# Kernel optimization log

Measured on AMD Instinct MI355X. Metric: run time of the kernel, lower is better.

The kernel has to match this reference:

```python
import jax, jax.numpy as jnp
import numpy as np

EXP_CLAMP = 1.0e6
DENOM_EPS = 1e-10
LRELU_ALPHA = 0.01


def setup_inputs() -> dict:
    key = jax.random.key(0)
    k1, k2, k3, k4, k5, k6 = jax.random.split(key, 6)
    B, N, E, F = 4, 16384, 262144, 64
    h = jax.random.normal(k1, (B, N, F), dtype=jnp.float32)
    edge = jax.random.randint(k2, (B, E, 2), 0, N, dtype=jnp.int32)
    edge_num = jax.random.randint(k3, (B,), 1, E, dtype=jnp.int32)
    edge_weight = jax.random.uniform(k4, (B, E), dtype=jnp.float32)
    W = jax.random.normal(k5, (F, F), dtype=jnp.float32) * 0.15  # xavier-ish scale
    a = jax.random.normal(k6, (1, 2 * F), dtype=jnp.float32) * 0.12
    return {"h": h, "edge": edge, "edge_num": edge_num,
            "edge_weight": edge_weight, "W": W, "a": a}


def _seg_sum(src, idx, num_segments):
    # src: [E, ...], idx: [E] -> [num_segments, ...]
    return jax.ops.segment_sum(src, idx, num_segments=num_segments)


def reference(h, edge, edge_num, edge_weight, W, a):
    B, N, Fin = h.shape
    E = edge.shape[1]
    # linear transform: Wh = h @ W^T  -> [B, N, Fout]
    Wh = jnp.einsum('bnf,of->bno', h, W)
    ctr = edge[:, :, 0]  # [B, E]
    nbr = edge[:, :, 1]  # [B, E]
    Wh_c = jnp.take_along_axis(Wh, ctr[:, :, None], axis=1)  # [B, E, Fout]
    Wh_n = jnp.take_along_axis(Wh, nbr[:, :, None], axis=1)  # [B, E, Fout]
    a_input = jnp.concatenate([Wh_c, Wh_n], axis=-1) * edge_weight[:, :, None]
    # attention logits: leakyrelu(a_input @ a^T), squeeze to [B, E]
    att1 = jax.nn.leaky_relu(jnp.einsum('bek,k->be', a_input, a[0]), LRELU_ALPHA)
    # per-batch valid-edge mask (edges beyond edge_num zeroed, as in torch loop)
    mask = (jnp.arange(E, dtype=jnp.int32)[None, :] < edge_num[:, None])
    x_exp = jnp.clip(jnp.exp(att1), 0.0, EXP_CLAMP) * mask.astype(att1.dtype)
    # segment softmax denominator over center nodes
    denom = DENOM_EPS + jax.vmap(_seg_sum, in_axes=(0, 0, None))(x_exp, ctr, N)  # [B, N]
    att = x_exp / jnp.take_along_axis(denom, ctr, axis=1)  # [B, E]
    # weighted neighbor aggregation via scatter-add on center index
    att_Wh = Wh_n * att[:, :, None]  # masked edges already have att == 0
    h_prime = jax.vmap(_seg_sum, in_axes=(0, 0, None))(att_Wh, ctr, N)  # [B, N, Fout]
    return jax.nn.relu(h_prime)
```

## Files before the change

### kernel.cpp

```cpp
#include <hip/hip_runtime.h>

#define BB 4
#define NN 16384
#define EE 262144
#define FF 64
#define ROWS (BB * NN)
#define CAP 64
#define CHUNKS 64
#define CHUNK_E (EE / CHUNKS)
#define TILE_R 256

typedef __bf16 bf16x8 __attribute__((ext_vector_type(8)));
typedef float  f32x4  __attribute__((ext_vector_type(4)));

__device__ __forceinline__ unsigned short f32_to_bf16(float f) {
    unsigned int u = __float_as_uint(f);
    u += 0x7FFFu + ((u >> 16) & 1u);
    return (unsigned short)(u >> 16);
}

__global__ __launch_bounds__(256) void mfma_kernel(
    const float* __restrict__ h, const float* __restrict__ W,
    const float* __restrict__ a,
    unsigned short* __restrict__ Wh,
    float* __restrict__ sc, float* __restrict__ sn)
{
    __shared__ float wc[FF], wn[FF];
    const int t = threadIdx.x;
    const int lane = t & 63;
    const int m = lane & 15;
    const int q = lane >> 4;

    if (t < 128) {
        const int f = t & 63;
        const float* av = a + (t >> 6) * FF;
        float s = 0.0f;
        #pragma unroll 8
        for (int o = 0; o < FF; ++o)
            s = fmaf(av[o], W[o * FF + f], s);
        (t < 64 ? wc : wn)[f] = s;
    }

    bf16x8 bfrag[4][2];
    #pragma unroll
    for (int nt = 0; nt < 4; ++nt) {
        const float* wr = W + (nt * 16 + m) * FF;
        #pragma unroll
        for (int kh = 0; kh < 2; ++kh) {
            const float4 v0 = *(const float4*)(wr + kh * 32 + q * 8);
            const float4 v1 = *(const float4*)(wr + kh * 32 + q * 8 + 4);
            bf16x8 b;
            b[0] = (__bf16)v0.x; b[1] = (__bf16)v0.y;
            b[2] = (__bf16)v0.z; b[3] = (__bf16)v0.w;
            b[4] = (__bf16)v1.x; b[5] = (__bf16)v1.y;
            b[6] = (__bf16)v1.z; b[7] = (__bf16)v1.w;
            bfrag[nt][kh] = b;
        }
    }

    __syncthreads();

    const int waveId = (blockIdx.x * 256 + t) >> 6;
    const int R0 = waveId * 16;
    const float* hr = h + (size_t)(R0 + m) * FF;
    bf16x8 af[2];
    float s1 = 0.0f, s2 = 0.0f;
    #pragma unroll
    for (int kh = 0; kh < 2; ++kh) {
        const float4 v0 = *(const float4*)(hr + kh * 32 + q * 8);
        const float4 v1 = *(const float4*)(hr + kh * 32 + q * 8 + 4);
        bf16x8 aa;
        aa[0] = (__bf16)v0.x; aa[1] = (__bf16)v0.y;
        aa[2] = (__bf16)v0.z; aa[3] = (__bf16)v0.w;
        aa[4] = (__bf16)v1.x; aa[5] = (__bf16)v1.y;
        aa[6] = (__bf16)v1.z; aa[7] = (__bf16)v1.w;
        af[kh] = aa;
        const int fb = kh * 32 + q * 8;
        const float4 c0 = *(const float4*)&wc[fb];
        const float4 c1 = *(const float4*)&wc[fb + 4];
        const float4 n0 = *(const float4*)&wn[fb];
        const float4 n1 = *(const float4*)&wn[fb + 4];
        s1 = fmaf(v0.x, c0.x, fmaf(v0.y, c0.y, fmaf(v0.z, c0.z, fmaf(v0.w, c0.w, s1))));
        s1 = fmaf(v1.x, c1.x, fmaf(v1.y, c1.y, fmaf(v1.z, c1.z, fmaf(v1.w, c1.w, s1))));
        s2 = fmaf(v0.x, n0.x, fmaf(v0.y, n0.y, fmaf(v0.z, n0.z, fmaf(v0.w, n0.w, s2))));
        s2 = fmaf(v1.x, n1.x, fmaf(v1.y, n1.y, fmaf(v1.z, n1.z, fmaf(v1.w, n1.w, s2))));
    }
    s1 += __shfl_xor(s1, 16); s2 += __shfl_xor(s2, 16);
    s1 += __shfl_xor(s1, 32); s2 += __shfl_xor(s2, 32);
    if (lane < 16) { sc[R0 + m] = s1; sn[R0 + m] = s2; }

    #pragma unroll
    for (int nt = 0; nt < 4; ++nt) {
        f32x4 acc = {0.f, 0.f, 0.f, 0.f};
        acc = __builtin_amdgcn_mfma_f32_16x16x32_bf16(af[0], bfrag[nt][0], acc, 0, 0, 0);
        acc = __builtin_amdgcn_mfma_f32_16x16x32_bf16(af[1], bfrag[nt][1], acc, 0, 0, 0);
        #pragma unroll
        for (int i = 0; i < 4; ++i)
            Wh[(size_t)(R0 + q * 4 + i) * FF + nt * 16 + m] = f32_to_bf16(acc[i]);
    }
}

__global__ __launch_bounds__(1024) void hist_kernel(
    const int* __restrict__ edge, const int* __restrict__ edge_num,
    unsigned short* __restrict__ histG)
{
    __shared__ unsigned int hist[NN];
    const int g = blockIdx.x;
    const int b = g >> 6, c = g & (CHUNKS - 1);
    const int t = threadIdx.x;
    const int en = edge_num[b];
    const int e0 = c * CHUNK_E;
    if (e0 >= en) return;

    for (int r = t; r < NN; r += 1024) hist[r] = 0u;
    __syncthreads();

    const int2* ep = (const int2*)edge + (size_t)b * EE + e0;
    const int nAct = min(en - e0, CHUNK_E);
    for (int j = t; j < nAct; j += 1024)
        atomicAdd(&hist[ep[j].x], 1u);
    __syncthreads();

    ushort2* out2 = (ushort2*)(histG + (size_t)g * NN);
    for (int r2 = t; r2 < NN / 2; r2 += 1024) {
        ushort2 v;
        v.x = (unsigned short)hist[2 * r2];
        v.y = (unsigned short)hist[2 * r2 + 1];
        out2[r2] = v;
    }
}

__global__ __launch_bounds__(256) void scan_kernel(
    const int* __restrict__ edge_num,
    unsigned short* __restrict__ histG, int* __restrict__ cnt)
{
    __shared__ unsigned short tile[CHUNKS][TILE_R];
    const int g = blockIdx.x;
    const int b = g >> 6, tl = g & 63;
    const int r0 = tl * TILE_R;
    const int t = threadIdx.x;
    const int en = edge_num[b];
    const int nact = min((en + CHUNK_E - 1) / CHUNK_E, CHUNKS);

    for (int c = 0; c < nact; ++c)
        tile[c][t] = histG[(size_t)(b * CHUNKS + c) * NN + r0 + t];
    __syncthreads();

    unsigned int acc = 0;
    for (int c = 0; c < nact; ++c) {
        const unsigned int v = tile[c][t];
        tile[c][t] = (unsigned short)(acc > 65535u ? 65535u : acc);
        acc += v;
    }
    cnt[b * NN + r0 + t] = (int)acc;

    for (int c = 0; c < nact; ++c)
        histG[(size_t)(b * CHUNKS + c) * NN + r0 + t] = tile[c][t];
}

__global__ __launch_bounds__(1024) void scatter_kernel(
    const int* __restrict__ edge, const int* __restrict__ edge_num,
    const unsigned short* __restrict__ baseG,
    const float* __restrict__ sc, const float* __restrict__ sn,
    const float* __restrict__ ew,
    unsigned int* __restrict__ payload)
{
    __shared__ unsigned int slotA[NN];
    const int g = blockIdx.x;
    const int b = g >> 6, c = g & (CHUNKS - 1);
    const int t = threadIdx.x;
    const int en = edge_num[b];
    const int e0 = c * CHUNK_E;
    if (e0 >= en) return;

    const ushort2* b2 = (const ushort2*)(baseG + (size_t)(b * CHUNKS + c) * NN);
    for (int r2 = t; r2 < NN / 2; r2 += 1024) {
        const ushort2 v = b2[r2];
        slotA[2 * r2]     = v.x;
        slotA[2 * r2 + 1] = v.y;
    }
    __syncthreads();

    const int2* ep = (const int2*)edge + (size_t)b * EE + e0;
    const int nAct = min(en - e0, CHUNK_E);
    const float* scB = sc + b * NN;
    const float* snB = sn + b * NN;
    const float* ewB = ew + (size_t)b * EE + e0;
    unsigned int* payB = payload + (size_t)b * NN * CAP;

    for (int j = t; j < nAct; j += 1024) {
        const int2 e2 = ep[j];
        const float w  = ewB[j];
        const float s0 = w * (scB[e2.x] + snB[e2.y]);
        const float s1 = s0 > 0.0f ? s0 : 0.01f * s0;
        const float xe = fminf(__expf(s1), 1000000.0f);
        const unsigned int slot = atomicAdd(&slotA[e2.x], 1u);
        if (slot < CAP)
            payB[(size_t)e2.x * CAP + slot] =
                ((__float_as_uint(xe) + 0x2000u) & 0xFFFFC000u) | (unsigned int)e2.y;
    }
}

__global__ __launch_bounds__(256) void gather_kernel(
    const int* __restrict__ cnt, const unsigned int* __restrict__ payload,
    const uint2* __restrict__ Wh2,
    float* __restrict__ out)
{
    const int bi = blockIdx.x;
    const int xcd = bi & 7;
    const int batch = xcd >> 1;
    const int within = ((bi >> 3) << 1) | (xcd & 1);
    const int w = threadIdx.x >> 6;
    const int lane = threadIdx.x & 63;
    const int r = lane >> 4;
    const int f = lane & 15;
    const int gbase = lane & 48;
    const int rq = within * 4 + w;
    const int row = batch * NN + rq * 4 + r;

    const unsigned int* pl = payload + (size_t)row * CAP;
    const uint2* WhB = Wh2 + (size_t)batch * NN * 16;

    int deg = cnt[row];
    unsigned int raw = pl[f];
    if (deg > CAP) deg = CAP;

    int jmax = deg;
    jmax = max(jmax, __shfl_xor(jmax, 16));
    jmax = max(jmax, __shfl_xor(jmax, 32));

    float a0 = 0.f, a1 = 0.f, a2 = 0.f, a3 = 0.f, pdsum = 0.f;

    for (int base = 0; base < jmax; base += 16) {
        const unsigned int p = (base + f < deg) ? raw : 0u;
        pdsum += __uint_as_float(p & 0xFFFFC000u);

        unsigned int rawN = 0u;
        if (base + 16 < jmax) rawN = pl[base + 16 + f];

        const int lim = min(16, jmax - base);
        for (int j4 = 0; j4 < lim; j4 += 4) {
            const unsigned int pv0 = __shfl(p, gbase + j4 + 0);
            const unsigned int pv1 = __shfl(p, gbase + j4 + 1);
            const unsigned int pv2 = __shfl(p, gbase + j4 + 2);
            const unsigned int pv3 = __shfl(p, gbase + j4 + 3);
            const uint2 w0 = WhB[(size_t)(pv0 & 0x3FFFu) * 16 + f];
            const uint2 w1 = WhB[(size_t)(pv1 & 0x3FFFu) * 16 + f];
            const uint2 w2 = WhB[(size_t)(pv2 & 0x3FFFu) * 16 + f];
            const uint2 w3 = WhB[(size_t)(pv3 & 0x3FFFu) * 16 + f];
            const float xe0 = __uint_as_float(pv0 & 0xFFFFC000u);
            const float xe1 = __uint_as_float(pv1 & 0xFFFFC000u);
            const float xe2 = __uint_as_float(pv2 & 0xFFFFC000u);
            const float xe3 = __uint_as_float(pv3 & 0xFFFFC000u);
            a0 = fmaf(xe0, __uint_as_float(w0.x << 16),         a0);
            a1 = fmaf(xe0, __uint_as_float(w0.x & 0xFFFF0000u), a1);
            a2 = fmaf(xe0, __uint_as_float(w0.y << 16),         a2);
            a3 = fmaf(xe0, __uint_as_float(w0.y & 0xFFFF0000u), a3);
            a0 = fmaf(xe1, __uint_as_float(w1.x << 16),         a0);
            a1 = fmaf(xe1, __uint_as_float(w1.x & 0xFFFF0000u), a1);
            a2 = fmaf(xe1, __uint_as_float(w1.y << 16),         a2);
            a3 = fmaf(xe1, __uint_as_float(w1.y & 0xFFFF0000u), a3);
            a0 = fmaf(xe2, __uint_as_float(w2.x << 16),         a0);
            a1 = fmaf(xe2, __uint_as_float(w2.x & 0xFFFF0000u), a1);
            a2 = fmaf(xe2, __uint_as_float(w2.y << 16),         a2);
            a3 = fmaf(xe2, __uint_as_float(w2.y & 0xFFFF0000u), a3);
            a0 = fmaf(xe3, __uint_as_float(w3.x << 16),         a0);
            a1 = fmaf(xe3, __uint_as_float(w3.x & 0xFFFF0000u), a1);
            a2 = fmaf(xe3, __uint_as_float(w3.y << 16),         a2);
            a3 = fmaf(xe3, __uint_as_float(w3.y & 0xFFFF0000u), a3);
        }
        raw = rawN;
    }

    pdsum += __shfl_xor(pdsum, 1);
    pdsum += __shfl_xor(pdsum, 2);
    pdsum += __shfl_xor(pdsum, 4);
    pdsum += __shfl_xor(pdsum, 8);

    const float inv = 1.0f / (1e-10f + pdsum);
    float4 o;
    o.x = fmaxf(a0 * inv, 0.0f);
    o.y = fmaxf(a1 * inv, 0.0f);
    o.z = fmaxf(a2 * inv, 0.0f);
    o.w = fmaxf(a3 * inv, 0.0f);
    ((float4*)out)[(size_t)row * 16 + f] = o;
}

extern "C" void kernel_launch(void* const* d_in, const int* in_sizes, int n_in,
                              void* d_out, int out_size, void* d_ws, size_t ws_size,
                              hipStream_t stream)
{
    const float* h        = (const float*)d_in[0];
    const int*   edge     = (const int*)  d_in[1];
    const int*   edge_num = (const int*)  d_in[2];
    const float* ew       = (const float*)d_in[3];
    const float* W        = (const float*)d_in[4];
    const float* a        = (const float*)d_in[5];
    float* out = (float*)d_out;

    unsigned short* Wh = (unsigned short*)d_ws;
    float* sc        = (float*)(Wh + (size_t)BB * NN * FF);
    float* sn        = sc + ROWS;
    int*   cnt       = (int*)(sn + ROWS);
    unsigned int* payload = (unsigned int*)(cnt + ROWS);
    unsigned short* histG = (unsigned short*)(payload + (size_t)ROWS * CAP);

    mfma_kernel<<<1024, 256, 0, stream>>>(h, W, a, Wh, sc, sn);

    hist_kernel<<<BB * CHUNKS, 1024, 0, stream>>>(edge, edge_num, histG);

    scan_kernel<<<BB * (NN / TILE_R), 256, 0, stream>>>(edge_num, histG, cnt);

    scatter_kernel<<<BB * CHUNKS, 1024, 0, stream>>>(edge, edge_num, histG,
                                                     sc, sn, ew, payload);

    gather_kernel<<<4096, 256, 0, stream>>>(cnt, payload,
                                            (const uint2*)Wh, out);
}
```

Baseline: 134.4 us.

## Fuse MFMA projection with edge histogram, double chunks, parallelize scan across chunk quarters

Merges the bf16 MFMA projection of Wh and the attention score terms with the per-chunk center-node histogram in one 1024-thread kernel. Waves 0-7 do the matmul while waves 8-15 clear the shared histogram, then all threads count edges. Edge chunks go from 64 to 128 per batch, so the histogram, scan and scatter grids double. The scan kernel now splits the chunk prefix into four 32-chunk quarters per 256-row tile to cut serial depth. This removes one launch and adds parallelism, but doubles histogram memory traffic and zero-fill work per chunk, and the 64 KB shared histogram lowers occupancy for the matmul.

```diff
diff --git a/kernel.cpp b/kernel.cpp
--- a/kernel.cpp
+++ b/kernel.cpp
@@ -6,7 +6,7 @@
 #define FF 64
 #define ROWS (BB * NN)
 #define CAP 64
-#define CHUNKS 64
+#define CHUNKS 128
 #define CHUNK_E (EE / CHUNKS)
 #define TILE_R 256
 
@@ -19,143 +19,158 @@
     return (unsigned short)(u >> 16);
 }
 
-__global__ __launch_bounds__(256) void mfma_kernel(
+__global__ __launch_bounds__(1024) void mfma_hist_kernel(
     const float* __restrict__ h, const float* __restrict__ W,
     const float* __restrict__ a,
+    const int* __restrict__ edge, const int* __restrict__ edge_num,
     unsigned short* __restrict__ Wh,
-    float* __restrict__ sc, float* __restrict__ sn)
+    float* __restrict__ sc, float* __restrict__ sn,
+    unsigned short* __restrict__ histG)
 {
     __shared__ float wc[FF], wn[FF];
+    __shared__ unsigned int hist[NN];
     const int t = threadIdx.x;
+    const int w = t >> 6;
     const int lane = t & 63;
     const int m = lane & 15;
     const int q = lane >> 4;
 
-    if (t < 128) {
-        const int f = t & 63;
-        const float* av = a + (t >> 6) * FF;
-        float s = 0.0f;
-        #pragma unroll 8
-        for (int o = 0; o < FF; ++o)
-            s = fmaf(av[o], W[o * FF + f], s);
-        (t < 64 ? wc : wn)[f] = s;
-    }
+    const int g = blockIdx.x;
+    const int b = g >> 7, c = g & (CHUNKS - 1);
+    const int en = edge_num[b];
+    const int e0 = c * CHUNK_E;
+    const bool active = (e0 < en);
 
     bf16x8 bfrag[4][2];
-    #pragma unroll
-    for (int nt = 0; nt < 4; ++nt) {
-        const float* wr = W + (nt * 16 + m) * FF;
+    if (w < 8) {
+        if (t < 128) {
+            const int f = t & 63;
+            const float* av = a + (t >> 6) * FF;
+            float s = 0.0f;
+            #pragma unroll 8
+            for (int o = 0; o < FF; ++o)
+                s = fmaf(av[o], W[o * FF + f], s);
+            (t < 64 ? wc : wn)[f] = s;
+        }
+        #pragma unroll
+        for (int nt = 0; nt < 4; ++nt) {
+            const float* wr = W + (nt * 16 + m) * FF;
+            #pragma unroll
+            for (int kh = 0; kh < 2; ++kh) {
+                const float4 v0 = *(const float4*)(wr + kh * 32 + q * 8);
+                const float4 v1 = *(const float4*)(wr + kh * 32 + q * 8 + 4);
+                bf16x8 bb;
+                bb[0] = (__bf16)v0.x; bb[1] = (__bf16)v0.y;
+                bb[2] = (__bf16)v0.z; bb[3] = (__bf16)v0.w;
+                bb[4] = (__bf16)v1.x; bb[5] = (__bf16)v1.y;
+                bb[6] = (__bf16)v1.z; bb[7] = (__bf16)v1.w;
+                bfrag[nt][kh] = bb;
+            }
+        }
+    } else if (active) {
+        for (int r = t - 512; r < NN; r += 512) hist[r] = 0u;
+    }
+    __syncthreads();
+
+    if (w < 8) {
+        const int waveId = g * 8 + w;
+        const int R0 = waveId * 16;
+        const float* hr = h + (size_t)(R0 + m) * FF;
+        bf16x8 af[2];
+        float s1 = 0.0f, s2 = 0.0f;
         #pragma unroll
         for (int kh = 0; kh < 2; ++kh) {
-            const float4 v0 = *(const float4*)(wr + kh * 32 + q * 8);
-            const float4 v1 = *(const float4*)(wr + kh * 32 + q * 8 + 4);
-            bf16x8 b;
-            b[0] = (__bf16)v0.x; b[1] = (__bf16)v0.y;
-            b[2] = (__bf16)v0.z; b[3] = (__bf16)v0.w;
-            b[4] = (__bf16)v1.x; b[5] = (__bf16)v1.y;
-            b[6] = (__bf16)v1.z; b[7] = (__bf16)v1.w;
-            bfrag[nt][kh] = b;
-        }
-    }
-
-    __syncthreads();
-
-    const int waveId = (blockIdx.x * 256 + t) >> 6;
-    const int R0 = waveId * 16;
-    const float* hr = h + (size_t)(R0 + m) * FF;
-    bf16x8 af[2];
-    float s1 = 0.0f, s2 = 0.0f;
-    #pragma unroll
-    for (int kh = 0; kh < 2; ++kh) {
-        const float4 v0 = *(const float4*)(hr + kh * 32 + q * 8);
-        const float4 v1 = *(const float4*)(hr + kh * 32 + q * 8 + 4);
-        bf16x8 aa;
-        aa[0] = (__bf16)v0.x; aa[1] = (__bf16)v0.y;
-        aa[2] = (__bf16)v0.z; aa[3] = (__bf16)v0.w;
-        aa[4] = (__bf16)v1.x; aa[5] = (__bf16)v1.y;
-        aa[6] = (__bf16)v1.z; aa[7] = (__bf16)v1.w;
-        af[kh] = aa;
-        const int fb = kh * 32 + q * 8;
-        const float4 c0 = *(const float4*)&wc[fb];
-        const float4 c1 = *(const float4*)&wc[fb + 4];
-        const float4 n0 = *(const float4*)&wn[fb];
-        const float4 n1 = *(const float4*)&wn[fb + 4];
-        s1 = fmaf(v0.x, c0.x, fmaf(v0.y, c0.y, fmaf(v0.z, c0.z, fmaf(v0.w, c0.w, s1))));
-        s1 = fmaf(v1.x, c1.x, fmaf(v1.y, c1.y, fmaf(v1.z, c1.z, fmaf(v1.w, c1.w, s1))));
-        s2 = fmaf(v0.x, n0.x, fmaf(v0.y, n0.y, fmaf(v0.z, n0.z, fmaf(v0.w, n0.w, s2))));
-        s2 = fmaf(v1.x, n1.x, fmaf(v1.y, n1.y, fmaf(v1.z, n1.z, fmaf(v1.w, n1.w, s2))));
-    }
-    s1 += __shfl_xor(s1, 16); s2 += __shfl_xor(s2, 16);
-    s1 += __shfl_xor(s1, 32); s2 += __shfl_xor(s2, 32);
-    if (lane < 16) { sc[R0 + m] = s1; sn[R0 + m] = s2; }
-
-    #pragma unroll
-    for (int nt = 0; nt < 4; ++nt) {
-        f32x4 acc = {0.f, 0.f, 0.f, 0.f};
-        acc = __builtin_amdgcn_mfma_f32_16x16x32_bf16(af[0], bfrag[nt][0], acc, 0, 0, 0);
-        acc = __builtin_amdgcn_mfma_f32_16x16x32_bf16(af[1], bfrag[nt][1], acc, 0, 0, 0);
+            const float4 v0 = *(const float4*)(hr + kh * 32 + q * 8);
+            const float4 v1 = *(const float4*)(hr + kh * 32 + q * 8 + 4);
+            bf16x8 aa;
+            aa[0] = (__bf16)v0.x; aa[1] = (__bf16)v0.y;
+            aa[2] = (__bf16)v0.z; aa[3] = (__bf16)v0.w;
+            aa[4] = (__bf16)v1.x; aa[5] = (__bf16)v1.y;
+            aa[6] = (__bf16)v1.z; aa[7] = (__bf16)v1.w;
+            af[kh] = aa;
+            const int fb = kh * 32 + q * 8;
+            const float4 c0 = *(const float4*)&wc[fb];
+            const float4 c1 = *(const float4*)&wc[fb + 4];
+            const float4 n0 = *(const float4*)&wn[fb];
+            const float4 n1 = *(const float4*)&wn[fb + 4];
+            s1 = fmaf(v0.x, c0.x, fmaf(v0.y, c0.y, fmaf(v0.z, c0.z, fmaf(v0.w, c0.w, s1))));
+            s1 = fmaf(v1.x, c1.x, fmaf(v1.y, c1.y, fmaf(v1.z, c1.z, fmaf(v1.w, c1.w, s1))));
+            s2 = fmaf(v0.x, n0.x, fmaf(v0.y, n0.y, fmaf(v0.z, n0.z, fmaf(v0.w, n0.w, s2))));
+            s2 = fmaf(v1.x, n1.x, fmaf(v1.y, n1.y, fmaf(v1.z, n1.z, fmaf(v1.w, n1.w, s2))));
+        }
+        s1 += __shfl_xor(s1, 16); s2 += __shfl_xor(s2, 16);
+        s1 += __shfl_xor(s1, 32); s2 += __shfl_xor(s2, 32);
+        if (lane < 16) { sc[R0 + m] = s1; sn[R0 + m] = s2; }
+
         #pragma unroll
-        for (int i = 0; i < 4; ++i)
-            Wh[(size_t)(R0 + q * 4 + i) * FF + nt * 16 + m] = f32_to_bf16(acc[i]);
-    }
-}
-
-__global__ __launch_bounds__(1024) void hist_kernel(
-    const int* __restrict__ edge, const int* __restrict__ edge_num,
-    unsigned short* __restrict__ histG)
-{
-    __shared__ unsigned int hist[NN];
-    const int g = blockIdx.x;
-    const int b = g >> 6, c = g & (CHUNKS - 1);
-    const int t = threadIdx.x;
-    const int en = edge_num[b];
-    const int e0 = c * CHUNK_E;
-    if (e0 >= en) return;
-
-    for (int r = t; r < NN; r += 1024) hist[r] = 0u;
-    __syncthreads();
-
-    const int2* ep = (const int2*)edge + (size_t)b * EE + e0;
-    const int nAct = min(en - e0, CHUNK_E);
-    for (int j = t; j < nAct; j += 1024)
-        atomicAdd(&hist[ep[j].x], 1u);
-    __syncthreads();
-
-    ushort2* out2 = (ushort2*)(histG + (size_t)g * NN);
-    for (int r2 = t; r2 < NN / 2; r2 += 1024) {
-        ushort2 v;
-        v.x = (unsigned short)hist[2 * r2];
-        v.y = (unsigned short)hist[2 * r2 + 1];
-        out2[r2] = v;
-    }
-}
-
-__global__ __launch_bounds__(256) void scan_kernel(
+        for (int nt = 0; nt < 4; ++nt) {
+            f32x4 acc = {0.f, 0.f, 0.f, 0.f};
+            acc = __builtin_amdgcn_mfma_f32_16x16x32_bf16(af[0], bfrag[nt][0], acc, 0, 0, 0);
+            acc = __builtin_amdgcn_mfma_f32_16x16x32_bf16(af[1], bfrag[nt][1], acc, 0, 0, 0);
+            #pragma unroll
+            for (int i = 0; i < 4; ++i)
+                Wh[(size_t)(R0 + q * 4 + i) * FF + nt * 16 + m] = f32_to_bf16(acc[i]);
+        }
+    }
+
+    if (active) {
+        const int2* ep = (const int2*)edge + (size_t)b * EE + e0;
+        const int nAct = min(en - e0, CHUNK_E);
+        for (int j = t; j < nAct; j += 1024)
+            atomicAdd(&hist[ep[j].x], 1u);
+        __syncthreads();
+
+        ushort2* out2 = (ushort2*)(histG + (size_t)g * NN);
+        for (int r2 = t; r2 < NN / 2; r2 += 1024) {
+            ushort2 v;
+            v.x = (unsigned short)hist[2 * r2];
+            v.y = (unsigned short)hist[2 * r2 + 1];
+            out2[r2] = v;
+        }
+    }
+}
+
+__global__ __launch_bounds__(1024) void scan_kernel(
     const int* __restrict__ edge_num,
     unsigned short* __restrict__ histG, int* __restrict__ cnt)
 {
     __shared__ unsigned short tile[CHUNKS][TILE_R];
+    __shared__ unsigned int qs[4][TILE_R];
     const int g = blockIdx.x;
     const int b = g >> 6, tl = g & 63;
     const int r0 = tl * TILE_R;
     const int t = threadIdx.x;
+    const int rr = t & 255;
+    const int qt = t >> 8;
     const int en = edge_num[b];
     const int nact = min((en + CHUNK_E - 1) / CHUNK_E, CHUNKS);
 
-    for (int c = 0; c < nact; ++c)
-        tile[c][t] = histG[(size_t)(b * CHUNKS + c) * NN + r0 + t];
+    const unsigned short* hb = histG + (size_t)(b * CHUNKS) * NN + r0;
+    unsigned int s = 0;
+    #pragma unroll 4
+    for (int c = qt * 32; c < qt * 32 + 32; ++c) {
+        const unsigned int v = (c < nact) ? (unsigned int)hb[(size_t)c * NN + rr] : 0u;
+        tile[c][rr] = (unsigned short)v;
+        s += v;
+    }
+    qs[qt][rr] = s;
     __syncthreads();
 
     unsigned int acc = 0;
-    for (int c = 0; c < nact; ++c) {
-        const unsigned int v = tile[c][t];
-        tile[c][t] = (unsigned short)(acc > 65535u ? 65535u : acc);
+    for (int qq = 0; qq < qt; ++qq) acc += qs[qq][rr];
+    #pragma unroll 4
+    for (int c = qt * 32; c < qt * 32 + 32; ++c) {
+        const unsigned int v = tile[c][rr];
+        tile[c][rr] = (unsigned short)(acc > 65535u ? 65535u : acc);
         acc += v;
     }
-    cnt[b * NN + r0 + t] = (int)acc;
-
-    for (int c = 0; c < nact; ++c)
-        histG[(size_t)(b * CHUNKS + c) * NN + r0 + t] = tile[c][t];
+    if (qt == 3) cnt[b * NN + r0 + rr] = (int)acc;
+    __syncthreads();
+
+    unsigned short* hbw = histG + (size_t)(b * CHUNKS) * NN + r0;
+    #pragma unroll 4
+    for (int c = qt * 32; c < qt * 32 + 32; ++c)
+        if (c < nact) hbw[(size_t)c * NN + rr] = tile[c][rr];
 }
 
 __global__ __launch_bounds__(1024) void scatter_kernel(
@@ -167,13 +182,13 @@
 {
     __shared__ unsigned int slotA[NN];
     const int g = blockIdx.x;
-    const int b = g >> 6, c = g & (CHUNKS - 1);
+    const int b = g >> 7, c = g & (CHUNKS - 1);
     const int t = threadIdx.x;
     const int en = edge_num[b];
     const int e0 = c * CHUNK_E;
     if (e0 >= en) return;
 
-    const ushort2* b2 = (const ushort2*)(baseG + (size_t)(b * CHUNKS + c) * NN);
+    const ushort2* b2 = (const ushort2*)(baseG + (size_t)g * NN);
     for (int r2 = t; r2 < NN / 2; r2 += 1024) {
         const ushort2 v = b2[r2];
         slotA[2 * r2]     = v.x;
@@ -190,8 +205,8 @@
 
     for (int j = t; j < nAct; j += 1024) {
         const int2 e2 = ep[j];
-        const float w  = ewB[j];
-        const float s0 = w * (scB[e2.x] + snB[e2.y]);
+        const float wgt = ewB[j];
+        const float s0 = wgt * (scB[e2.x] + snB[e2.y]);
         const float s1 = s0 > 0.0f ? s0 : 0.01f * s0;
         const float xe = fminf(__expf(s1), 1000000.0f);
         const unsigned int slot = atomicAdd(&slotA[e2.x], 1u);
@@ -305,11 +320,10 @@
     unsigned int* payload = (unsigned int*)(cnt + ROWS);
     unsigned short* histG = (unsigned short*)(payload + (size_t)ROWS * CAP);
 
-    mfma_kernel<<<1024, 256, 0, stream>>>(h, W, a, Wh, sc, sn);
-
-    hist_kernel<<<BB * CHUNKS, 1024, 0, stream>>>(edge, edge_num, histG);
-
-    scan_kernel<<<BB * (NN / TILE_R), 256, 0, stream>>>(edge_num, histG, cnt);
+    mfma_hist_kernel<<<BB * CHUNKS, 1024, 0, stream>>>(h, W, a, edge, edge_num,
+                                                       Wh, sc, sn, histG);
+
+    scan_kernel<<<BB * (NN / TILE_R), 1024, 0, stream>>>(edge_num, histG, cnt);
 
     scatter_kernel<<<BB * CHUNKS, 1024, 0, stream>>>(edge, edge_num, histG,
                                                      sc, sn, ew, payload);
```

Result: slower. 140.8 us (+4.7%).

## Replace histogram/scan/scatter pipeline with single node-range binning kernel

Applied to the files above, without the earlier changes.

Three kernels (per-chunk histogram, cross-chunk scan, scatter) are replaced by one bin_kernel. Each block owns a 256-node range of center indices, streams the whole edge list of its batch, and keeps only edges whose center falls in its range, using LDS counters for slot assignment. This removes two launches and the global histogram round trips. In exchange every block rereads all edges of its batch, 64x redundant edge traffic though mostly from L2. Slot order within a row is no longer deterministic by chunk, so summation order may vary.

```diff
diff --git a/kernel.cpp b/kernel.cpp
--- a/kernel.cpp
+++ b/kernel.cpp
@@ -6,9 +6,8 @@
 #define FF 64
 #define ROWS (BB * NN)
 #define CAP 64
-#define CHUNKS 64
-#define CHUNK_E (EE / CHUNKS)
-#define TILE_R 256
+#define NSPLIT 64
+#define SPLIT_R (NN / NSPLIT)
 
 typedef __bf16 bf16x8 __attribute__((ext_vector_type(8)));
 typedef float  f32x4  __attribute__((ext_vector_type(4)));
@@ -100,105 +99,61 @@
     }
 }
 
-__global__ __launch_bounds__(1024) void hist_kernel(
+__global__ __launch_bounds__(1024) void bin_kernel(
     const int* __restrict__ edge, const int* __restrict__ edge_num,
-    unsigned short* __restrict__ histG)
-{
-    __shared__ unsigned int hist[NN];
-    const int g = blockIdx.x;
-    const int b = g >> 6, c = g & (CHUNKS - 1);
+    const float* __restrict__ ew,
+    const float* __restrict__ sc, const float* __restrict__ sn,
+    unsigned int* __restrict__ payload, int* __restrict__ cnt)
+{
+    __shared__ float scL[SPLIT_R];
+    __shared__ unsigned int ctr[SPLIT_R];
+    const int bi = blockIdx.x;
+    const int xcd = bi & 7;
+    const int b = xcd >> 1;
+    const int split = ((bi >> 3) << 1) | (xcd & 1);
+    const int r0 = split * SPLIT_R;
     const int t = threadIdx.x;
+
+    if (t < SPLIT_R) {
+        scL[t] = sc[b * NN + r0 + t];
+        ctr[t] = 0u;
+    }
+    __syncthreads();
+
     const int en = edge_num[b];
-    const int e0 = c * CHUNK_E;
-    if (e0 >= en) return;
-
-    for (int r = t; r < NN; r += 1024) hist[r] = 0u;
+    const int n4 = (en + 1) >> 1;
+    const int4* ep4 = (const int4*)(edge + (size_t)b * EE * 2);
+    const float* ewB = ew + (size_t)b * EE;
+    const float* snB = sn + b * NN;
+    unsigned int* payB = payload + (size_t)b * NN * CAP;
+    const int lo = r0, hi = r0 + SPLIT_R;
+
+    for (int i4 = t; i4 < n4; i4 += 1024) {
+        const int4 e4 = ep4[i4];
+        if (e4.x >= lo && e4.x < hi) {
+            const float w  = ewB[2 * i4];
+            const float s0 = w * (scL[e4.x - lo] + snB[e4.y]);
+            const float s1 = s0 > 0.0f ? s0 : 0.01f * s0;
+            const float xe = fminf(__expf(s1), 1000000.0f);
+            const unsigned int slot = atomicAdd(&ctr[e4.x - lo], 1u);
+            if (slot < CAP)
+                payB[(size_t)e4.x * CAP + slot] =
+                    ((__float_as_uint(xe) + 0x2000u) & 0xFFFFC000u) | (unsigned int)e4.y;
+        }
+        if (2 * i4 + 1 < en && e4.z >= lo && e4.z < hi) {
+            const float w  = ewB[2 * i4 + 1];
+            const float s0 = w * (scL[e4.z - lo] + snB[e4.w]);
+            const float s1 = s0 > 0.0f ? s0 : 0.01f * s0;
+            const float xe = fminf(__expf(s1), 1000000.0f);
+            const unsigned int slot = atomicAdd(&ctr[e4.z - lo], 1u);
+            if (slot < CAP)
+                payB[(size_t)e4.z * CAP + slot] =
+                    ((__float_as_uint(xe) + 0x2000u) & 0xFFFFC000u) | (unsigned int)e4.w;
+        }
+    }
     __syncthreads();
 
-    const int2* ep = (const int2*)edge + (size_t)b * EE + e0;
-    const int nAct = min(en - e0, CHUNK_E);
-    for (int j = t; j < nAct; j += 1024)
-        atomicAdd(&hist[ep[j].x], 1u);
-    __syncthreads();
-
-    ushort2* out2 = (ushort2*)(histG + (size_t)g * NN);
-    for (int r2 = t; r2 < NN / 2; r2 += 1024) {
-        ushort2 v;
-        v.x = (unsigned short)hist[2 * r2];
-        v.y = (unsigned short)hist[2 * r2 + 1];
-        out2[r2] = v;
-    }
-}
-
-__global__ __launch_bounds__(256) void scan_kernel(
-    const int* __restrict__ edge_num,
-    unsigned short* __restrict__ histG, int* __restrict__ cnt)
-{
-    __shared__ unsigned short tile[CHUNKS][TILE_R];
-    const int g = blockIdx.x;
-    const int b = g >> 6, tl = g & 63;
-    const int r0 = tl * TILE_R;
-    const int t = threadIdx.x;
-    const int en = edge_num[b];
-    const int nact = min((en + CHUNK_E - 1) / CHUNK_E, CHUNKS);
-
-    for (int c = 0; c < nact; ++c)
-        tile[c][t] = histG[(size_t)(b * CHUNKS + c) * NN + r0 + t];
-    __syncthreads();
-
-    unsigned int acc = 0;
-    for (int c = 0; c < nact; ++c) {
-        const unsigned int v = tile[c][t];
-        tile[c][t] = (unsigned short)(acc > 65535u ? 65535u : acc);
-        acc += v;
-    }
-    cnt[b * NN + r0 + t] = (int)acc;
-
-    for (int c = 0; c < nact; ++c)
-        histG[(size_t)(b * CHUNKS + c) * NN + r0 + t] = tile[c][t];
-}
-
-__global__ __launch_bounds__(1024) void scatter_kernel(
-    const int* __restrict__ edge, const int* __restrict__ edge_num,
-    const unsigned short* __restrict__ baseG,
-    const float* __restrict__ sc, const float* __restrict__ sn,
-    const float* __restrict__ ew,
-    unsigned int* __restrict__ payload)
-{
-    __shared__ unsigned int slotA[NN];
-    const int g = blockIdx.x;
-    const int b = g >> 6, c = g & (CHUNKS - 1);
-    const int t = threadIdx.x;
-    const int en = edge_num[b];
-    const int e0 = c * CHUNK_E;
-    if (e0 >= en) return;
-
-    const ushort2* b2 = (const ushort2*)(baseG + (size_t)(b * CHUNKS + c) * NN);
-    for (int r2 = t; r2 < NN / 2; r2 += 1024) {
-        const ushort2 v = b2[r2];
-        slotA[2 * r2]     = v.x;
-        slotA[2 * r2 + 1] = v.y;
-    }
-    __syncthreads();
-
-    const int2* ep = (const int2*)edge + (size_t)b * EE + e0;
-    const int nAct = min(en - e0, CHUNK_E);
-    const float* scB = sc + b * NN;
-    const float* snB = sn + b * NN;
-    const float* ewB = ew + (size_t)b * EE + e0;
-    unsigned int* payB = payload + (size_t)b * NN * CAP;
-
-    for (int j = t; j < nAct; j += 1024) {
-        const int2 e2 = ep[j];
-        const float w  = ewB[j];
-        const float s0 = w * (scB[e2.x] + snB[e2.y]);
-        const float s1 = s0 > 0.0f ? s0 : 0.01f * s0;
-        const float xe = fminf(__expf(s1), 1000000.0f);
-        const unsigned int slot = atomicAdd(&slotA[e2.x], 1u);
-        if (slot < CAP)
-            payB[(size_t)e2.x * CAP + slot] =
-                ((__float_as_uint(xe) + 0x2000u) & 0xFFFFC000u) | (unsigned int)e2.y;
-    }
+    if (t < SPLIT_R) cnt[b * NN + r0 + t] = (int)ctr[t];
 }
 
 __global__ __launch_bounds__(256) void gather_kernel(
@@ -303,16 +258,11 @@
     float* sn        = sc + ROWS;
     int*   cnt       = (int*)(sn + ROWS);
     unsigned int* payload = (unsigned int*)(cnt + ROWS);
-    unsigned short* histG = (unsigned short*)(payload + (size_t)ROWS * CAP);
 
     mfma_kernel<<<1024, 256, 0, stream>>>(h, W, a, Wh, sc, sn);
 
-    hist_kernel<<<BB * CHUNKS, 1024, 0, stream>>>(edge, edge_num, histG);
-
-    scan_kernel<<<BB * (NN / TILE_R), 256, 0, stream>>>(edge_num, histG, cnt);
-
-    scatter_kernel<<<BB * CHUNKS, 1024, 0, stream>>>(edge, edge_num, histG,
-                                                     sc, sn, ew, payload);
+    bin_kernel<<<256, 1024, 0, stream>>>(edge, edge_num, ew, sc, sn,
+                                         payload, cnt);
 
     gather_kernel<<<4096, 256, 0, stream>>>(cnt, payload,
                                             (const uint2*)Wh, out);
```

Result: slower. 193.5 us (+44.0%).

## Split hist and scatter blocks by center-node half to double grid and cache scores in LDS

Applied to the files above, without the earlier changes.

The hist and scatter kernels now launch two blocks per (batch, chunk), each owning half the center-node range. That halves the LDS histogram/slot arrays and doubles the number of blocks, which should improve occupancy and parallelism. Scatter also stages the half's center scores in LDS, so those reads no longer go to global memory. The cost is that every block reads the full edge chunk and discards edges outside its half, so edge-read traffic doubles.

```diff
diff --git a/kernel.cpp b/kernel.cpp
--- a/kernel.cpp
+++ b/kernel.cpp
@@ -9,6 +9,7 @@
 #define CHUNKS 64
 #define CHUNK_E (EE / CHUNKS)
 #define TILE_R 256
+#define HALF_R (NN / 2)
 
 typedef __bf16 bf16x8 __attribute__((ext_vector_type(8)));
 typedef float  f32x4  __attribute__((ext_vector_type(4)));
@@ -104,25 +105,30 @@
     const int* __restrict__ edge, const int* __restrict__ edge_num,
     unsigned short* __restrict__ histG)
 {
-    __shared__ unsigned int hist[NN];
+    __shared__ unsigned int hist[HALF_R];
     const int g = blockIdx.x;
-    const int b = g >> 6, c = g & (CHUNKS - 1);
+    const int half = g & 1;
+    const int c = (g >> 1) & (CHUNKS - 1);
+    const int b = g >> 7;
     const int t = threadIdx.x;
     const int en = edge_num[b];
     const int e0 = c * CHUNK_E;
     if (e0 >= en) return;
 
-    for (int r = t; r < NN; r += 1024) hist[r] = 0u;
+    for (int r = t; r < HALF_R; r += 1024) hist[r] = 0u;
     __syncthreads();
 
     const int2* ep = (const int2*)edge + (size_t)b * EE + e0;
     const int nAct = min(en - e0, CHUNK_E);
-    for (int j = t; j < nAct; j += 1024)
-        atomicAdd(&hist[ep[j].x], 1u);
-    __syncthreads();
-
-    ushort2* out2 = (ushort2*)(histG + (size_t)g * NN);
-    for (int r2 = t; r2 < NN / 2; r2 += 1024) {
+    for (int j = t; j < nAct; j += 1024) {
+        const int2 e2 = ep[j];
+        if ((e2.x >> 13) == half)
+            atomicAdd(&hist[e2.x & (HALF_R - 1)], 1u);
+    }
+    __syncthreads();
+
+    ushort2* out2 = (ushort2*)(histG + (size_t)(b * CHUNKS + c) * NN + half * HALF_R);
+    for (int r2 = t; r2 < HALF_R / 2; r2 += 1024) {
         ushort2 v;
         v.x = (unsigned short)hist[2 * r2];
         v.y = (unsigned short)hist[2 * r2 + 1];
@@ -165,36 +171,44 @@
     const float* __restrict__ ew,
     unsigned int* __restrict__ payload)
 {
-    __shared__ unsigned int slotA[NN];
+    __shared__ unsigned int slotA[HALF_R];
+    __shared__ float scL[HALF_R];
     const int g = blockIdx.x;
-    const int b = g >> 6, c = g & (CHUNKS - 1);
+    const int half = g & 1;
+    const int c = (g >> 1) & (CHUNKS - 1);
+    const int b = g >> 7;
     const int t = threadIdx.x;
     const int en = edge_num[b];
     const int e0 = c * CHUNK_E;
     if (e0 >= en) return;
 
-    const ushort2* b2 = (const ushort2*)(baseG + (size_t)(b * CHUNKS + c) * NN);
-    for (int r2 = t; r2 < NN / 2; r2 += 1024) {
+    const int rbase = half * HALF_R;
+    const ushort2* b2 = (const ushort2*)(baseG + (size_t)(b * CHUNKS + c) * NN + rbase);
+    for (int r2 = t; r2 < HALF_R / 2; r2 += 1024) {
         const ushort2 v = b2[r2];
         slotA[2 * r2]     = v.x;
         slotA[2 * r2 + 1] = v.y;
     }
+    const float* scH = sc + b * NN + rbase;
+    for (int r = t; r < HALF_R; r += 1024)
+        scL[r] = scH[r];
     __syncthreads();
 
     const int2* ep = (const int2*)edge + (size_t)b * EE + e0;
     const int nAct = min(en - e0, CHUNK_E);
-    const float* scB = sc + b * NN;
     const float* snB = sn + b * NN;
     const float* ewB = ew + (size_t)b * EE + e0;
     unsigned int* payB = payload + (size_t)b * NN * CAP;
 
     for (int j = t; j < nAct; j += 1024) {
         const int2 e2 = ep[j];
-        const float w  = ewB[j];
-        const float s0 = w * (scB[e2.x] + snB[e2.y]);
+        if ((e2.x >> 13) != half) continue;
+        const int rl = e2.x & (HALF_R - 1);
+        const float wgt = ewB[j];
+        const float s0 = wgt * (scL[rl] + snB[e2.y]);
         const float s1 = s0 > 0.0f ? s0 : 0.01f * s0;
         const float xe = fminf(__expf(s1), 1000000.0f);
-        const unsigned int slot = atomicAdd(&slotA[e2.x], 1u);
+        const unsigned int slot = atomicAdd(&slotA[rl], 1u);
         if (slot < CAP)
             payB[(size_t)e2.x * CAP + slot] =
                 ((__float_as_uint(xe) + 0x2000u) & 0xFFFFC000u) | (unsigned int)e2.y;
@@ -307,12 +321,12 @@
 
     mfma_kernel<<<1024, 256, 0, stream>>>(h, W, a, Wh, sc, sn);
 
-    hist_kernel<<<BB * CHUNKS, 1024, 0, stream>>>(edge, edge_num, histG);
+    hist_kernel<<<BB * CHUNKS * 2, 1024, 0, stream>>>(edge, edge_num, histG);
 
     scan_kernel<<<BB * (NN / TILE_R), 256, 0, stream>>>(edge_num, histG, cnt);
 
-    scatter_kernel<<<BB * CHUNKS, 1024, 0, stream>>>(edge, edge_num, histG,
-                                                     sc, sn, ew, payload);
+    scatter_kernel<<<BB * CHUNKS * 2, 1024, 0, stream>>>(edge, edge_num, histG,
+                                                         sc, sn, ew, payload);
 
     gather_kernel<<<4096, 256, 0, stream>>>(cnt, payload,
                                             (const uint2*)Wh, out);
```

New measurement: 130.3 us. 1.03x faster.
